# Kernel tuning notes

Hardware: AMD Instinct MI355X
Metric: run time of the kernel (lower is better)

Reference implementation:

```python
import jax, jax.numpy as jnp
import numpy as np

NUM_HEADS = 8
NEG_SLOPE = 0.2


def setup_inputs() -> dict:
    key = jax.random.key(0)
    k1, k2, k3, k4 = jax.random.split(key, 4)
    B, N, D_IN, D_K, D_V = 4, 4096, 256, 256, 256
    x = jax.random.normal(k1, (B, N, D_IN), dtype=jnp.float32)
    Wq = jax.random.normal(k2, (D_IN, D_K), dtype=jnp.float32) * (1.0 / np.sqrt(D_IN))
    Wk = jax.random.normal(k3, (D_IN, D_K), dtype=jnp.float32) * (1.0 / np.sqrt(D_IN))
    Wv = jax.random.normal(k4, (D_IN, D_V), dtype=jnp.float32) * (1.0 / np.sqrt(D_IN))
    return {"x": x, "Wq": Wq, "Wk": Wk, "Wv": Wv}


def reference(x, Wq, Wk, Wv):
    B, N, _ = x.shape
    nh = NUM_HEADS
    dim_k = Wq.shape[1]
    dim_v = Wv.shape[1]
    dk, dv = dim_k // nh, dim_v // nh
    nor_fact = 1.0 / np.sqrt(dk)
    # project and split heads: [B, H, N, dk]
    q = (x @ Wq).reshape(B, N, nh, dk).transpose(0, 2, 1, 3)
    k = (x @ Wk).reshape(B, N, nh, dk).transpose(0, 2, 1, 3)
    v = (x @ Wv).reshape(B, N, nh, dv).transpose(0, 2, 1, 3)
    # all-pairs scores, scaled then LeakyReLU (no softmax)
    dist = jnp.einsum('bhnd,bhmd->bhnm', q, k) * nor_fact
    dist = jnp.where(dist >= 0, dist, NEG_SLOPE * dist)
    att = jnp.einsum('bhnm,bhmd->bhnd', dist, v)
    return att.transpose(0, 2, 1, 3).reshape(B, N, dim_v)
```

## Files before the change

kernel.cpp:

```cpp
#include <hip/hip_runtime.h>

typedef __attribute__((ext_vector_type(8))) short short8;
typedef __attribute__((ext_vector_type(4))) short short4v;
typedef __attribute__((ext_vector_type(4))) float f32x4;
typedef __attribute__((ext_vector_type(16))) float f32x16;
typedef __attribute__((ext_vector_type(2))) unsigned int u32x2;

#define MFMA16x32(A, B, C) \
  __builtin_amdgcn_mfma_f32_16x16x32_bf16((A), (B), (C), 0, 0, 0)
#define MFMA32x16(A, B, C) \
  __builtin_amdgcn_mfma_f32_32x32x16_bf16((A), (B), (C), 0, 0, 0)

#if defined(__has_builtin)
#if __has_builtin(__builtin_amdgcn_mfma_f32_32x32x8bf16_1k)
#define HAVE_32X8 1
#endif
#endif
__device__ __forceinline__ f32x16 mfma32x8(short4v a, short4v b, f32x16 c) {
#ifdef HAVE_32X8
  return __builtin_amdgcn_mfma_f32_32x32x8bf16_1k(a, b, c, 0, 0, 0);
#else
  f32x16 d;
  asm("v_mfma_f32_32x32x8_bf16 %0, %1, %2, %3"
      : "=v"(d)
      : "v"(a), "v"(b), "v"(c));
  return d;
#endif
}

__device__ __forceinline__ void async_cp16(const unsigned short* g, void* l) {
  __builtin_amdgcn_global_load_lds(
      (const __attribute__((address_space(1))) unsigned int*)g,
      (__attribute__((address_space(3))) unsigned int*)l, 16, 0, 0);
}

__device__ __forceinline__ unsigned int fbits(float f) {
  return __builtin_bit_cast(unsigned int, f);
}
__device__ __forceinline__ unsigned int pack_bf16(float a, float b) {
  return __builtin_amdgcn_perm(fbits(b), fbits(a), 0x07060302u);
}
__device__ __forceinline__ unsigned short bf16_rne(float f) {
  unsigned int u = fbits(f);
  return (unsigned short)((u + 0x8000u) >> 16);
}
__device__ __forceinline__ float lk(float x) { return fmaxf(x, 0.2f * x); }

__global__ __launch_bounds__(256) void prep_kernel(
    const float* __restrict__ x, const float* __restrict__ Wq,
    const float* __restrict__ Wk, const float* __restrict__ Wv,
    unsigned short* __restrict__ xb, unsigned short* __restrict__ WT) {
  const int bid = blockIdx.x;
  if (bid < 4096) {
    const size_t i = ((size_t)bid * 256 + threadIdx.x) * 4;
    const float4 f = *(const float4*)(x + i);
    u32x2 u = {
        (unsigned int)bf16_rne(f.x) | ((unsigned int)bf16_rne(f.y) << 16),
        (unsigned int)bf16_rne(f.z) | ((unsigned int)bf16_rne(f.w) << 16)};
    *(u32x2*)(xb + i) = u;
    return;
  }
  __shared__ float tile[32][33];
  const int wb = bid - 4096;
  const int g = wb / 64, rem = wb % 64;
  const int k0 = (rem >> 3) * 32, n0 = (rem & 7) * 32;
  const float* W = (g == 0) ? Wq : (g == 1) ? Wk : Wv;
  const int t = threadIdx.x;
  {
    const int kr = t >> 3, nc = (t & 7) * 4;
    const float4 f = *(const float4*)(W + (size_t)(k0 + kr) * 256 + n0 + nc);
    tile[kr][nc + 0] = f.x; tile[kr][nc + 1] = f.y;
    tile[kr][nc + 2] = f.z; tile[kr][nc + 3] = f.w;
  }
  __syncthreads();
  {
    const int nr = t >> 3, kc = (t & 7) * 4;
    unsigned int u0 = (unsigned int)bf16_rne(tile[kc + 0][nr]) |
                      ((unsigned int)bf16_rne(tile[kc + 1][nr]) << 16);
    unsigned int u1 = (unsigned int)bf16_rne(tile[kc + 2][nr]) |
                      ((unsigned int)bf16_rne(tile[kc + 3][nr]) << 16);
    u32x2 u = {u0, u1};
    *(u32x2*)(WT + (size_t)g * 65536 + (size_t)(n0 + nr) * 256 + k0 + kc) = u;
  }
}

__global__ __launch_bounds__(256, 2) void proj_kernel(
    const unsigned short* __restrict__ xb, const unsigned short* __restrict__ WT,
    unsigned short* __restrict__ QH, unsigned short* __restrict__ KH,
    unsigned short* __restrict__ VT) {
  __shared__ __align__(16) char smem[65536];
  const int tid = threadIdx.x;
  const int w = tid >> 6, lane = tid & 63, l15 = lane & 15, quad = lane >> 4;
  const int bid = blockIdx.x;
  const int mtile = bid / 6, nt = bid % 6;
  const int g = nt >> 1, n0 = (nt & 1) * 128;
  const int m0 = mtile * 128;

  const int srow = lane >> 3, useg = lane & 7;
  const int swz = (useg ^ srow) * 8;
  const unsigned short* aSj[4];
  const unsigned short* bSj[4];
#pragma unroll
  for (int j = 0; j < 4; j++) {
    aSj[j] = xb + (size_t)(m0 + w * 32 + j * 8 + srow) * 256 + swz;
    bSj[j] = WT + (size_t)g * 65536 +
             (size_t)(n0 + w * 32 + j * 8 + srow) * 256 + swz;
  }

#pragma unroll
  for (int j = 0; j < 4; j++) {
    async_cp16(aSj[j], smem + w * 4096 + j * 1024);
    async_cp16(bSj[j], smem + 16384 + w * 4096 + j * 1024);
  }
  __syncthreads();

  const f32x4 zero = {0.f, 0.f, 0.f, 0.f};
  f32x4 acc[2][8];
#pragma unroll
  for (int s = 0; s < 2; s++)
#pragma unroll
    for (int c = 0; c < 8; c++) acc[s][c] = zero;

  const int sega = ((quad) ^ (l15 & 7)) * 16;
  int aoff[2], boff[8];
#pragma unroll
  for (int s = 0; s < 2; s++) aoff[s] = (w * 32 + s * 16 + l15) * 128;
#pragma unroll
  for (int c = 0; c < 8; c++) boff[c] = 16384 + (c * 16 + l15) * 128;

#pragma unroll
  for (int t = 0; t < 4; t++) {
    const int nb = t & 1;
    const int kn = ((t + 1) & 3) * 64;
#pragma unroll
    for (int j = 0; j < 4; j++) {
      async_cp16(aSj[j] + kn, smem + (nb ^ 1) * 32768 + w * 4096 + j * 1024);
      async_cp16(bSj[j] + kn,
                 smem + (nb ^ 1) * 32768 + 16384 + w * 4096 + j * 1024);
    }
#pragma unroll
    for (int ks = 0; ks < 2; ks++) {
      const int sg = ks ? (sega ^ 64) : sega;
      short8 af[2], bf[8];
#pragma unroll
      for (int s = 0; s < 2; s++)
        af[s] = *(const short8*)(smem + nb * 32768 + aoff[s] + sg);
#pragma unroll
      for (int c = 0; c < 8; c++)
        bf[c] = *(const short8*)(smem + nb * 32768 + boff[c] + sg);
      if (g < 2) {
#pragma unroll
        for (int s = 0; s < 2; s++)
#pragma unroll
          for (int c = 0; c < 8; c++)
            acc[s][c] = MFMA16x32(bf[c], af[s], acc[s][c]);
      } else {
#pragma unroll
        for (int s = 0; s < 2; s++)
#pragma unroll
          for (int c = 0; c < 8; c++)
            acc[s][c] = MFMA16x32(af[s], bf[c], acc[s][c]);
      }
    }
    __syncthreads();
  }

  if (g < 2) {
    unsigned short* O = g ? KH : QH;
    const float sc = g ? 1.0f : 0.17677669529663688f;
#pragma unroll
    for (int s = 0; s < 2; s++)
#pragma unroll
      for (int c = 0; c < 8; c++) {
        const int row = m0 + w * 32 + s * 16 + l15;
        const int col = n0 + c * 16 + quad * 4;
        const int bb = row >> 12, nn = row & 4095;
        const int hh = col >> 5, dl = col & 31;
        u32x2 pk = {pack_bf16(acc[s][c][0] * sc, acc[s][c][1] * sc),
                    pack_bf16(acc[s][c][2] * sc, acc[s][c][3] * sc)};
        *(u32x2*)(O + ((size_t)(bb * 8 + hh) * 4096 + nn) * 32 + dl) = pk;
      }
  } else {
#pragma unroll
    for (int s = 0; s < 2; s++)
#pragma unroll
      for (int c = 0; c < 8; c++) {
        const int col = n0 + c * 16 + l15;
        const int hh = col >> 5, dl = col & 31;
        const int row = m0 + w * 32 + s * 16 + quad * 4;
        const int bb = row >> 12, nn = row & 4095;
        u32x2 pk = {pack_bf16(acc[s][c][0], acc[s][c][1]),
                    pack_bf16(acc[s][c][2], acc[s][c][3])};
        *(u32x2*)(VT + (size_t)((bb * 8 + hh) * 32 + dl) * 4096 + nn) = pk;
      }
  }
}

__global__ __launch_bounds__(256, 2) void attn_kernel(
    const unsigned short* __restrict__ QH, const unsigned short* __restrict__ KH,
    const unsigned short* __restrict__ VT, float* __restrict__ out) {
  __shared__ __align__(16) char smem[16384];
  const int tid = threadIdx.x;
  const int w = tid >> 6, lane = tid & 63, l31 = lane & 31, half = lane >> 5;
  const int bid = blockIdx.x;
  const int bh = bid & 31, qt = bid >> 5;
  const int b = bh >> 3, h = bh & 7;
  const int qbase = qt * 256 + w * 64;

  const unsigned short* Qp = QH + ((size_t)bh * 4096 + qbase + l31) * 32 + half * 8;
  short8 qf[2][2];
#pragma unroll
  for (int qg = 0; qg < 2; qg++)
#pragma unroll
    for (int kh = 0; kh < 2; kh++)
      qf[qg][kh] = *(const short8*)(Qp + qg * 1024 + kh * 16);

  const unsigned short* gK =
      KH + ((size_t)bh * 4096 + w * 16 + (lane >> 2)) * 32 + (lane & 3) * 8;
  const int vd = w * 8 + (lane >> 3);
  const unsigned short* gV =
      VT + ((size_t)bh * 32 + vd) * 4096 + ((lane & 7) ^ (vd & 7)) * 8;

  const int kbase = l31 * 64 + half * 16;
  int voff[8];
#pragma unroll
  for (int kk = 0; kk < 8; kk++)
    voff[kk] = 4096 + l31 * 128 + ((kk ^ (l31 & 7)) * 16) + half * 8;

  async_cp16(gK, smem + w * 1024);
  async_cp16(gV, smem + 4096 + w * 1024);
  gK += 2048;
  gV += 64;
  __syncthreads();

  f32x16 z16;
  f32x16 acc[2];
#pragma unroll
  for (int i = 0; i < 16; i++) { z16[i] = 0.f; acc[0][i] = 0.f; acc[1][i] = 0.f; }

#define ATTN_BODY(B_)                                                         \
  {                                                                           \
    async_cp16(gK, smem + ((B_) ^ 1) * 8192 + w * 1024);                      \
    async_cp16(gV, smem + ((B_) ^ 1) * 8192 + 4096 + w * 1024);               \
    gK += 2048;                                                               \
    gV += 64;                                                                 \
    short8 kf[2][2];                                                          \
    _Pragma("unroll") for (int kt = 0; kt < 2; kt++)                          \
        _Pragma("unroll") for (int kh = 0; kh < 2; kh++) kf[kt][kh] =         \
        *(const short8*)(smem + (B_)*8192 + kbase + kt * 2048 + kh * 32);     \
    short4v vf[8];                                                            \
    _Pragma("unroll") for (int kk = 0; kk < 8; kk++) vf[kk] =                 \
        *(const short4v*)(smem + (B_)*8192 + voff[kk]);                       \
    _Pragma("unroll") for (int qg = 0; qg < 2; qg++) {                        \
      _Pragma("unroll") for (int kt = 0; kt < 2; kt++) {                      \
        f32x16 st = MFMA32x16(kf[kt][0], qf[qg][0], z16);                     \
        st = MFMA32x16(kf[kt][1], qf[qg][1], st);                             \
        _Pragma("unroll") for (int g = 0; g < 4; g++) {                       \
          u32x2 pk = {pack_bf16(lk(st[4 * g + 0]), lk(st[4 * g + 1])),        \
                      pack_bf16(lk(st[4 * g + 2]), lk(st[4 * g + 3]))};       \
          acc[qg] =                                                           \
              mfma32x8(vf[kt * 4 + g], __builtin_bit_cast(short4v, pk),       \
                       acc[qg]);                                              \
        }                                                                     \
      }                                                                       \
    }                                                                         \
    __syncthreads();                                                          \
  }

  for (int it = 0; it < 64; it += 2) {
    ATTN_BODY(0)
    ATTN_BODY(1)
  }
#undef ATTN_BODY

#pragma unroll
  for (int qg = 0; qg < 2; qg++)
#pragma unroll
    for (int g = 0; g < 4; g++) {
      f32x4 o = {acc[qg][4 * g + 0], acc[qg][4 * g + 1], acc[qg][4 * g + 2],
                 acc[qg][4 * g + 3]};
      *(f32x4*)(out + ((size_t)b * 4096 + qbase + qg * 32 + l31) * 256 +
                h * 32 + g * 8 + half * 4) = o;
    }
}

extern "C" void kernel_launch(void* const* d_in, const int* in_sizes, int n_in,
                              void* d_out, int out_size, void* d_ws,
                              size_t ws_size, hipStream_t stream) {
  const float* x = (const float*)d_in[0];
  const float* Wq = (const float*)d_in[1];
  const float* Wk = (const float*)d_in[2];
  const float* Wv = (const float*)d_in[3];
  float* out = (float*)d_out;

  unsigned short* ws = (unsigned short*)d_ws;
  unsigned short* QHb = ws;
  unsigned short* KHb = ws + 4194304;
  unsigned short* VTb = ws + 2 * 4194304;
  unsigned short* xbb = ws + 3 * 4194304;
  unsigned short* WTb = ws + 4 * 4194304;

  prep_kernel<<<4288, 256, 0, stream>>>(x, Wq, Wk, Wv, xbb, WTb);
  proj_kernel<<<768, 256, 0, stream>>>(xbb, WTb, QHb, KHb, VTb);
  attn_kernel<<<512, 256, 0, stream>>>(QHb, KHb, VTb, out);
}
```

Measured before the change: 186.6 us.

## Retile attention kernel to 32 queries per wave with larger K/V stages

```diff
diff --git a/kernel.cpp b/kernel.cpp
--- a/kernel.cpp
+++ b/kernel.cpp
@@ -196,92 +196,95 @@
   }
 }
 
-__global__ __launch_bounds__(256, 2) void attn_kernel(
+__global__ __launch_bounds__(256, 4) void attn_kernel(
     const unsigned short* __restrict__ QH, const unsigned short* __restrict__ KH,
     const unsigned short* __restrict__ VT, float* __restrict__ out) {
-  __shared__ __align__(16) char smem[16384];
+  constexpr int VREG = 8192;
+  constexpr int BUF = 8192 + 8 * 1040;
+  __shared__ __align__(16) char smem[2 * BUF];
   const int tid = threadIdx.x;
   const int w = tid >> 6, lane = tid & 63, l31 = lane & 31, half = lane >> 5;
   const int bid = blockIdx.x;
   const int bh = bid & 31, qt = bid >> 5;
   const int b = bh >> 3, h = bh & 7;
-  const int qbase = qt * 256 + w * 64;
-
-  const unsigned short* Qp = QH + ((size_t)bh * 4096 + qbase + l31) * 32 + half * 8;
-  short8 qf[2][2];
-#pragma unroll
-  for (int qg = 0; qg < 2; qg++)
-#pragma unroll
-    for (int kh = 0; kh < 2; kh++)
-      qf[qg][kh] = *(const short8*)(Qp + qg * 1024 + kh * 16);
-
-  const unsigned short* gK =
-      KH + ((size_t)bh * 4096 + w * 16 + (lane >> 2)) * 32 + (lane & 3) * 8;
-  const int vd = w * 8 + (lane >> 3);
-  const unsigned short* gV =
-      VT + ((size_t)bh * 32 + vd) * 4096 + ((lane & 7) ^ (vd & 7)) * 8;
-
-  const int kbase = l31 * 64 + half * 16;
-  int voff[8];
-#pragma unroll
-  for (int kk = 0; kk < 8; kk++)
-    voff[kk] = 4096 + l31 * 128 + ((kk ^ (l31 & 7)) * 16) + half * 8;
-
-  async_cp16(gK, smem + w * 1024);
-  async_cp16(gV, smem + 4096 + w * 1024);
-  gK += 2048;
-  gV += 64;
+  const int qbase = qt * 128 + w * 32;
+
+  const unsigned short* Qp =
+      QH + ((size_t)bh * 4096 + qbase + l31) * 32 + half * 8;
+  short8 qf[2];
+  qf[0] = *(const short8*)(Qp);
+  qf[1] = *(const short8*)(Qp + 16);
+
+  const int key0 = (w * 128 + lane) >> 2, sl0 = lane & 3;
+  const unsigned short* gK0 =
+      KH + ((size_t)bh * 4096 + key0) * 32 + (sl0 ^ (key0 & 3)) * 8;
+  const unsigned short* gK1 = gK0 + 16 * 32;
+  const int d0 = w * 8 + (lane >> 4);
+  const int sv = lane & 15;
+  const unsigned short* gV0 = VT + ((size_t)bh * 32 + d0) * 4096 + sv * 8;
+  const unsigned short* gV1 = gV0 + 4 * 4096;
+  const int ldsK = w * 2048;
+  const int ldsV0 = VREG + (w * 2) * 1040;
+  const int ldsV1 = VREG + (w * 2 + 1) * 1040;
+
+  const int kb0 = l31 * 64 + ((half ^ (l31 & 3)) * 16);
+  const int kb1 = kb0 ^ 32;
+  const int vb = VREG + l31 * 256 + (l31 >> 2) * 16 + half * 8;
+
+  async_cp16(gK0, smem + ldsK);
+  async_cp16(gK1, smem + ldsK + 1024);
+  async_cp16(gV0, smem + ldsV0);
+  async_cp16(gV1, smem + ldsV1);
+  gK0 += 4096;
+  gK1 += 4096;
+  gV0 += 128;
+  gV1 += 128;
   __syncthreads();
 
-  f32x16 z16;
-  f32x16 acc[2];
-#pragma unroll
-  for (int i = 0; i < 16; i++) { z16[i] = 0.f; acc[0][i] = 0.f; acc[1][i] = 0.f; }
+  f32x16 z16, acc;
+#pragma unroll
+  for (int i = 0; i < 16; i++) { z16[i] = 0.f; acc[i] = 0.f; }
 
 #define ATTN_BODY(B_)                                                         \
   {                                                                           \
-    async_cp16(gK, smem + ((B_) ^ 1) * 8192 + w * 1024);                      \
-    async_cp16(gV, smem + ((B_) ^ 1) * 8192 + 4096 + w * 1024);               \
-    gK += 2048;                                                               \
-    gV += 64;                                                                 \
-    short8 kf[2][2];                                                          \
-    _Pragma("unroll") for (int kt = 0; kt < 2; kt++)                          \
-        _Pragma("unroll") for (int kh = 0; kh < 2; kh++) kf[kt][kh] =         \
-        *(const short8*)(smem + (B_)*8192 + kbase + kt * 2048 + kh * 32);     \
-    short4v vf[8];                                                            \
-    _Pragma("unroll") for (int kk = 0; kk < 8; kk++) vf[kk] =                 \
-        *(const short4v*)(smem + (B_)*8192 + voff[kk]);                       \
-    _Pragma("unroll") for (int qg = 0; qg < 2; qg++) {                        \
-      _Pragma("unroll") for (int kt = 0; kt < 2; kt++) {                      \
-        f32x16 st = MFMA32x16(kf[kt][0], qf[qg][0], z16);                     \
-        st = MFMA32x16(kf[kt][1], qf[qg][1], st);                             \
-        _Pragma("unroll") for (int g = 0; g < 4; g++) {                       \
-          u32x2 pk = {pack_bf16(lk(st[4 * g + 0]), lk(st[4 * g + 1])),        \
-                      pack_bf16(lk(st[4 * g + 2]), lk(st[4 * g + 3]))};       \
-          acc[qg] =                                                           \
-              mfma32x8(vf[kt * 4 + g], __builtin_bit_cast(short4v, pk),       \
-                       acc[qg]);                                              \
-        }                                                                     \
+    async_cp16(gK0, smem + ((B_) ^ 1) * BUF + ldsK);                          \
+    async_cp16(gK1, smem + ((B_) ^ 1) * BUF + ldsK + 1024);                   \
+    async_cp16(gV0, smem + ((B_) ^ 1) * BUF + ldsV0);                         \
+    async_cp16(gV1, smem + ((B_) ^ 1) * BUF + ldsV1);                         \
+    gK0 += 4096;                                                              \
+    gK1 += 4096;                                                              \
+    gV0 += 128;                                                               \
+    gV1 += 128;                                                               \
+    const char* Bc = smem + (B_)*BUF;                                         \
+    _Pragma("unroll") for (int kt = 0; kt < 4; kt++) {                        \
+      short8 kf0 = *(const short8*)(Bc + kt * 2048 + kb0);                    \
+      short8 kf1 = *(const short8*)(Bc + kt * 2048 + kb1);                    \
+      short4v vf[4];                                                          \
+      _Pragma("unroll") for (int g = 0; g < 4; g++) vf[g] =                   \
+          *(const short4v*)(Bc + vb + (kt * 4 + g) * 16);                     \
+      f32x16 st = MFMA32x16(kf0, qf[0], z16);                                 \
+      st = MFMA32x16(kf1, qf[1], st);                                         \
+      _Pragma("unroll") for (int g = 0; g < 4; g++) {                         \
+        u32x2 pk = {pack_bf16(lk(st[4 * g + 0]), lk(st[4 * g + 1])),          \
+                    pack_bf16(lk(st[4 * g + 2]), lk(st[4 * g + 3]))};         \
+        acc = mfma32x8(vf[g], __builtin_bit_cast(short4v, pk), acc);          \
       }                                                                       \
     }                                                                         \
     __syncthreads();                                                          \
   }
 
-  for (int it = 0; it < 64; it += 2) {
+  for (int it = 0; it < 32; it += 2) {
     ATTN_BODY(0)
     ATTN_BODY(1)
   }
 #undef ATTN_BODY
 
 #pragma unroll
-  for (int qg = 0; qg < 2; qg++)
-#pragma unroll
-    for (int g = 0; g < 4; g++) {
-      f32x4 o = {acc[qg][4 * g + 0], acc[qg][4 * g + 1], acc[qg][4 * g + 2],
-                 acc[qg][4 * g + 3]};
-      *(f32x4*)(out + ((size_t)b * 4096 + qbase + qg * 32 + l31) * 256 +
-                h * 32 + g * 8 + half * 4) = o;
-    }
+  for (int g = 0; g < 4; g++) {
+    f32x4 o = {acc[4 * g + 0], acc[4 * g + 1], acc[4 * g + 2], acc[4 * g + 3]};
+    *(f32x4*)(out + ((size_t)b * 4096 + qbase + l31) * 256 + h * 32 + g * 8 +
+              half * 4) = o;
+  }
 }
 
 extern "C" void kernel_launch(void* const* d_in, const int* in_sizes, int n_in,
@@ -302,5 +305,5 @@
 
   prep_kernel<<<4288, 256, 0, stream>>>(x, Wq, Wk, Wv, xbb, WTb);
   proj_kernel<<<768, 256, 0, stream>>>(xbb, WTb, QHb, KHb, VTb);
-  attn_kernel<<<512, 256, 0, stream>>>(QHb, KHb, VTb, out);
-}
+  attn_kernel<<<1024, 256, 0, stream>>>(QHb, KHb, VTb, out);
+}
```

Result: slower. 193.5 us (+3.7%).

## Double key tile per stage to 128 keys with swizzled K LDS layout

Applied to the files above, without the earlier changes.

```diff
diff --git a/kernel.cpp b/kernel.cpp
--- a/kernel.cpp
+++ b/kernel.cpp
@@ -199,7 +199,9 @@
 __global__ __launch_bounds__(256, 2) void attn_kernel(
     const unsigned short* __restrict__ QH, const unsigned short* __restrict__ KH,
     const unsigned short* __restrict__ VT, float* __restrict__ out) {
-  __shared__ __align__(16) char smem[16384];
+  constexpr int VREG = 8192;
+  constexpr int BUF = 16384;
+  __shared__ __align__(16) char smem[2 * BUF];
   const int tid = threadIdx.x;
   const int w = tid >> 6, lane = tid & 63, l31 = lane & 31, half = lane >> 5;
   const int bid = blockIdx.x;
@@ -207,7 +209,8 @@
   const int b = bh >> 3, h = bh & 7;
   const int qbase = qt * 256 + w * 64;
 
-  const unsigned short* Qp = QH + ((size_t)bh * 4096 + qbase + l31) * 32 + half * 8;
+  const unsigned short* Qp =
+      QH + ((size_t)bh * 4096 + qbase + l31) * 32 + half * 8;
   short8 qf[2][2];
 #pragma unroll
   for (int qg = 0; qg < 2; qg++)
@@ -215,59 +218,74 @@
     for (int kh = 0; kh < 2; kh++)
       qf[qg][kh] = *(const short8*)(Qp + qg * 1024 + kh * 16);
 
-  const unsigned short* gK =
-      KH + ((size_t)bh * 4096 + w * 16 + (lane >> 2)) * 32 + (lane & 3) * 8;
-  const int vd = w * 8 + (lane >> 3);
-  const unsigned short* gV =
-      VT + ((size_t)bh * 32 + vd) * 4096 + ((lane & 7) ^ (vd & 7)) * 8;
-
-  const int kbase = l31 * 64 + half * 16;
-  int voff[8];
-#pragma unroll
-  for (int kk = 0; kk < 8; kk++)
-    voff[kk] = 4096 + l31 * 128 + ((kk ^ (l31 & 7)) * 16) + half * 8;
-
-  async_cp16(gK, smem + w * 1024);
-  async_cp16(gV, smem + 4096 + w * 1024);
-  gK += 2048;
-  gV += 64;
+  const int klin = w * 128 + lane;
+  const int key0 = klin >> 2, p0 = klin & 3;
+  const unsigned short* gK0 =
+      KH + ((size_t)bh * 4096 + key0) * 32 + (p0 ^ ((key0 >> 1) & 3)) * 8;
+  const unsigned short* gK1 = gK0 + 16 * 32;
+  const int vlin0 = w * 128 + lane;
+  const int vd0 = vlin0 >> 4, vb0 = vlin0 & 15;
+  const unsigned short* gV0 =
+      VT + ((size_t)bh * 32 + vd0) * 4096 + (vb0 ^ (vd0 & 7)) * 8;
+  const int vlin1 = vlin0 + 64;
+  const int vd1 = vlin1 >> 4, vb1 = vlin1 & 15;
+  const unsigned short* gV1 =
+      VT + ((size_t)bh * 32 + vd1) * 4096 + (vb1 ^ (vd1 & 7)) * 8;
+  const int ldsK0 = w * 2048, ldsK1 = w * 2048 + 1024;
+  const int ldsV0 = VREG + w * 2048, ldsV1 = VREG + w * 2048 + 1024;
+
+  const int kb0 = l31 * 64 + ((half ^ ((l31 >> 1) & 3)) * 16);
+  const int kb1 = kb0 ^ 32;
+  const char* ptrK0 = (const char*)smem + kb0;
+  const char* ptrK1 = (const char*)smem + kb1;
+  const char* ptrV[8];
+#pragma unroll
+  for (int j = 0; j < 8; j++)
+    ptrV[j] = (const char*)smem + VREG + l31 * 256 + ((j ^ (l31 & 7)) * 16) +
+              half * 8;
+
+  async_cp16(gK0, smem + ldsK0);
+  async_cp16(gK1, smem + ldsK1);
+  async_cp16(gV0, smem + ldsV0);
+  async_cp16(gV1, smem + ldsV1);
+  gK0 += 4096; gK1 += 4096;
+  gV0 += 128;  gV1 += 128;
   __syncthreads();
 
-  f32x16 z16;
-  f32x16 acc[2];
+  f32x16 z16, acc[2];
 #pragma unroll
   for (int i = 0; i < 16; i++) { z16[i] = 0.f; acc[0][i] = 0.f; acc[1][i] = 0.f; }
 
 #define ATTN_BODY(B_)                                                         \
   {                                                                           \
-    async_cp16(gK, smem + ((B_) ^ 1) * 8192 + w * 1024);                      \
-    async_cp16(gV, smem + ((B_) ^ 1) * 8192 + 4096 + w * 1024);               \
-    gK += 2048;                                                               \
-    gV += 64;                                                                 \
-    short8 kf[2][2];                                                          \
-    _Pragma("unroll") for (int kt = 0; kt < 2; kt++)                          \
-        _Pragma("unroll") for (int kh = 0; kh < 2; kh++) kf[kt][kh] =         \
-        *(const short8*)(smem + (B_)*8192 + kbase + kt * 2048 + kh * 32);     \
-    short4v vf[8];                                                            \
-    _Pragma("unroll") for (int kk = 0; kk < 8; kk++) vf[kk] =                 \
-        *(const short4v*)(smem + (B_)*8192 + voff[kk]);                       \
-    _Pragma("unroll") for (int qg = 0; qg < 2; qg++) {                        \
-      _Pragma("unroll") for (int kt = 0; kt < 2; kt++) {                      \
-        f32x16 st = MFMA32x16(kf[kt][0], qf[qg][0], z16);                     \
-        st = MFMA32x16(kf[kt][1], qf[qg][1], st);                             \
+    async_cp16(gK0, smem + ((B_) ^ 1) * BUF + ldsK0);                         \
+    async_cp16(gK1, smem + ((B_) ^ 1) * BUF + ldsK1);                         \
+    async_cp16(gV0, smem + ((B_) ^ 1) * BUF + ldsV0);                         \
+    async_cp16(gV1, smem + ((B_) ^ 1) * BUF + ldsV1);                         \
+    gK0 += 4096; gK1 += 4096; gV0 += 128; gV1 += 128;                         \
+    _Pragma("unroll") for (int kt = 0; kt < 4; kt++) {                        \
+      short8 kf0 = *(const short8*)(ptrK0 + (B_)*BUF + kt * 2048);            \
+      short8 kf1 = *(const short8*)(ptrK1 + (B_)*BUF + kt * 2048);            \
+      short4v vf[4];                                                          \
+      _Pragma("unroll") for (int g = 0; g < 4; g++) {                         \
+        const int c = kt * 4 + g;                                             \
+        vf[g] = *(const short4v*)(ptrV[c & 7] + (B_)*BUF + (c >> 3) * 128);   \
+      }                                                                       \
+      _Pragma("unroll") for (int qg = 0; qg < 2; qg++) {                      \
+        f32x16 st = MFMA32x16(kf0, qf[qg][0], z16);                           \
+        st = MFMA32x16(kf1, qf[qg][1], st);                                   \
         _Pragma("unroll") for (int g = 0; g < 4; g++) {                       \
           u32x2 pk = {pack_bf16(lk(st[4 * g + 0]), lk(st[4 * g + 1])),        \
                       pack_bf16(lk(st[4 * g + 2]), lk(st[4 * g + 3]))};       \
-          acc[qg] =                                                           \
-              mfma32x8(vf[kt * 4 + g], __builtin_bit_cast(short4v, pk),       \
-                       acc[qg]);                                              \
+          acc[qg] = mfma32x8(vf[g], __builtin_bit_cast(short4v, pk),          \
+                             acc[qg]);                                        \
         }                                                                     \
       }                                                                       \
     }                                                                         \
     __syncthreads();                                                          \
   }
 
-  for (int it = 0; it < 64; it += 2) {
+  for (int it = 0; it < 32; it += 2) {
     ATTN_BODY(0)
     ATTN_BODY(1)
   }
```

Result: no change. 184.3 us (-1.2%).
